# Kernel tuning notes

Hardware: AMD Instinct MI355X
Metric: run time of the kernel (lower is better)

The kernel has to match this reference:

```python
import jax, jax.numpy as jnp
import numpy as np

BATCH, SEQ_LEN, VEC_DIM, WIDTH = 64, 256, 512, 3


def setup_inputs() -> dict:
    key = jax.random.key(0)
    k = jax.random.split(key, 8)
    F0r = jax.random.normal(k[0], (BATCH, SEQ_LEN, VEC_DIM), jnp.float32)
    F1r = jax.random.normal(k[1], (BATCH, SEQ_LEN, VEC_DIM), jnp.float32)
    sent0_mask = (jax.random.uniform(k[2], (BATCH, SEQ_LEN)) < 0.9).astype(jnp.float32)
    sent1_mask = (jax.random.uniform(k[3], (BATCH, SEQ_LEN)) < 0.9).astype(jnp.float32)
    # nn.Parameter(torch.randn(seq_len, vec_dim))
    W0 = jax.random.normal(k[4], (SEQ_LEN, VEC_DIM), jnp.float32)
    W1 = jax.random.normal(k[5], (SEQ_LEN, VEC_DIM), jnp.float32)
    # Conv2d(2, 1, kernel_size=(WIDTH, 1)) default init: U(-1/sqrt(fan_in), +)
    bound = 1.0 / np.sqrt(2 * WIDTH * 1)
    conv_w = jax.random.uniform(k[6], (1, 2, WIDTH, 1), jnp.float32, -bound, bound)
    conv_b = jax.random.uniform(k[7], (1,), jnp.float32, -bound, bound)
    return dict(F0r=F0r, F1r=F1r, sent0_mask=sent0_mask, sent1_mask=sent1_mask,
                W0=W0, W1=W1, conv_w=conv_w, conv_b=conv_b)


def _conv_tanh_pool(x, conv_w, conv_b):
    # x: [B, 2, S, D]; conv pad (WIDTH-1, 0) -> [B, 1, S+WIDTH-1, D]
    y = jax.lax.conv_general_dilated(
        x, conv_w, window_strides=(1, 1),
        padding=((WIDTH - 1, WIDTH - 1), (0, 0)),
        dimension_numbers=('NCHW', 'OIHW', 'NCHW'))
    y = jnp.tanh(y + conv_b[None, :, None, None])
    # AvgPool2d kernel (WIDTH,1), stride 1 -> [B, 1, S, D]
    y = jax.lax.reduce_window(y, 0.0, jax.lax.add,
                              (1, 1, WIDTH, 1), (1, 1, 1, 1), 'VALID') / WIDTH
    return y[:, 0]  # squeeze channel -> [B, S, D]


def reference(F0r, F1r, sent0_mask, sent1_mask, W0, W1, conv_w, conv_b):
    # masking is in-place in the torch code, so masked F0/F1 feed the conv too
    F0 = F0r * sent0_mask[:, :, None]  # [B, S, D]
    F1 = F1r * sent1_mask[:, :, None]
    # pairwise L2 via ||u-v||^2 = ||u||^2 + ||v||^2 - 2 u.v (avoids [B,S,S,D])
    sq0 = jnp.sum(F0 * F0, axis=-1)  # [B, S]
    sq1 = jnp.sum(F1 * F1, axis=-1)
    cross = jnp.einsum('bid,bjd->bij', F0, F1)  # [B, S, S]
    d2 = jnp.maximum(sq0[:, :, None] + sq1[:, None, :] - 2.0 * cross, 0.0)
    norm = jnp.where(d2 > 0, jnp.sqrt(jnp.where(d2 > 0, d2, 1.0)), 0.0)
    A = 1.0 / (1.0 + norm)  # [B, S, S]
    F0a = jnp.einsum('bij,id->bjd', A, W0)  # A^T @ W0
    F1a = jnp.einsum('bij,jd->bid', A, W1)  # A @ W1
    x0 = jnp.stack([F0, F0a], axis=1)  # [B, 2, S, D]
    x1 = jnp.stack([F1, F1a], axis=1)
    out0 = _conv_tanh_pool(x0, conv_w, conv_b)
    out1 = _conv_tanh_pool(x1, conv_w, conv_b)
    return out0, out1
```

## Files before the change

kernel.cpp:

```cpp
#include <hip/hip_runtime.h>

typedef unsigned short u16;
typedef __attribute__((ext_vector_type(8))) short short8;
typedef __attribute__((ext_vector_type(4))) float f32x4;

__device__ inline u16 f2bf(float f) {
    union { float f; unsigned u; } v; v.f = f;
    unsigned u = v.u;
    unsigned r = (u + 0x7FFFu + ((u >> 16) & 1u)) >> 16;
    return (u16)r;
}
__device__ inline float bf2f(u16 h) {
    union { unsigned u; float f; } v; v.u = ((unsigned)h) << 16;
    return v.f;
}
__device__ inline float ftanh(float x) {
    float e = __expf(2.f * x);
    return 1.f - 2.f / (e + 1.f);
}

__global__ __launch_bounds__(128) void prep_kernel(
    const float* __restrict__ F0r, const float* __restrict__ F1r,
    const float* __restrict__ m0, const float* __restrict__ m1,
    u16* __restrict__ F0b, u16* __restrict__ F1b,
    float* __restrict__ sq0, float* __restrict__ sq1)
{
    int bs = blockIdx.x;
    int t = threadIdx.x;
    size_t base = (size_t)bs * 512 + t * 4;
    float mk0 = m0[bs], mk1 = m1[bs];
    float4 v0 = *(const float4*)(F0r + base);
    float4 v1 = *(const float4*)(F1r + base);
    v0.x *= mk0; v0.y *= mk0; v0.z *= mk0; v0.w *= mk0;
    v1.x *= mk1; v1.y *= mk1; v1.z *= mk1; v1.w *= mk1;
    ushort4 u0; u0.x = f2bf(v0.x); u0.y = f2bf(v0.y); u0.z = f2bf(v0.z); u0.w = f2bf(v0.w);
    ushort4 u1; u1.x = f2bf(v1.x); u1.y = f2bf(v1.y); u1.z = f2bf(v1.z); u1.w = f2bf(v1.w);
    *(ushort4*)(F0b + base) = u0;
    *(ushort4*)(F1b + base) = u1;
    float s0p = v0.x*v0.x + v0.y*v0.y + v0.z*v0.z + v0.w*v0.w;
    float s1p = v1.x*v1.x + v1.y*v1.y + v1.z*v1.z + v1.w*v1.w;
    #pragma unroll
    for (int off = 32; off > 0; off >>= 1) {
        s0p += __shfl_xor(s0p, off);
        s1p += __shfl_xor(s1p, off);
    }
    __shared__ float red0[2], red1[2];
    if ((t & 63) == 0) { red0[t >> 6] = s0p; red1[t >> 6] = s1p; }
    __syncthreads();
    if (t == 0) { sq0[bs] = red0[0] + red0[1]; sq1[bs] = red1[0] + red1[1]; }
}

__global__ __launch_bounds__(256) void wtrans_kernel(
    const float* __restrict__ W0, const float* __restrict__ W1,
    u16* __restrict__ WT0, u16* __restrict__ WT1)
{
    int idx = blockIdx.x * 256 + threadIdx.x;
    int a = idx >> 17;
    int r = idx & 131071;
    int s = r >> 9, d = r & 511;
    const float* W = a ? W1 : W0;
    u16* WT = a ? WT1 : WT0;
    WT[d * 256 + s] = f2bf(W[r]);
}

__device__ inline void gemm128_core(
    const u16* __restrict__ Ap, int lda,
    const u16* __restrict__ Bp, int ldb,
    int K, int m0, int n0,
    u16 (*As)[72], u16 (*Bs)[72],
    f32x4 acc[4][4])
{
    const int t = threadIdx.x;
    const int lane = t & 63, w = t >> 6;
    const int wm = w >> 1, wn = w & 1;
    const int q = lane >> 4, lm = lane & 15;

    for (int k0 = 0; k0 < K; k0 += 64) {
        #pragma unroll
        for (int i = 0; i < 4; ++i) {
            int idx = i * 256 + t;
            int row = idx >> 3;
            int seg = idx & 7;
            *(uint4*)&As[row][seg * 8] =
                *(const uint4*)(Ap + (size_t)(m0 + row) * lda + k0 + seg * 8);
            *(uint4*)&Bs[row][seg * 8] =
                *(const uint4*)(Bp + (size_t)(n0 + row) * ldb + k0 + seg * 8);
        }
        __syncthreads();
        #pragma unroll
        for (int ks = 0; ks < 64; ks += 32) {
            short8 af[4], bfr[4];
            #pragma unroll
            for (int x = 0; x < 4; ++x) {
                af[x]  = *(const short8*)&As[wm * 64 + x * 16 + lm][ks + q * 8];
                bfr[x] = *(const short8*)&Bs[wn * 64 + x * 16 + lm][ks + q * 8];
            }
            #pragma unroll
            for (int x = 0; x < 4; ++x)
                #pragma unroll
                for (int y = 0; y < 4; ++y)
                    acc[x][y] = __builtin_amdgcn_mfma_f32_16x16x32_bf16(
                        af[x], bfr[y], acc[x][y], 0, 0, 0);
        }
        __syncthreads();
    }
}

__global__ __launch_bounds__(256) void gemm_cross_kernel(
    const u16* __restrict__ F0b, const u16* __restrict__ F1b,
    const float* __restrict__ sq0, const float* __restrict__ sq1,
    u16* __restrict__ Abf, u16* __restrict__ ATbf)
{
    __shared__ __align__(16) u16 As[128][72];
    __shared__ __align__(16) u16 Bs[128][72];
    int b = blockIdx.y, var = blockIdx.z;
    int m0 = (blockIdx.x >> 1) * 128, n0 = (blockIdx.x & 1) * 128;
    const u16 *Ap, *Bp; const float *sqR, *sqC; u16* Out;
    if (var == 0) {
        Ap = F0b + (size_t)b * 131072; Bp = F1b + (size_t)b * 131072;
        sqR = sq0 + b * 256; sqC = sq1 + b * 256;
        Out = Abf + (size_t)b * 65536;
    } else {
        Ap = F1b + (size_t)b * 131072; Bp = F0b + (size_t)b * 131072;
        sqR = sq1 + b * 256; sqC = sq0 + b * 256;
        Out = ATbf + (size_t)b * 65536;
    }
    f32x4 acc[4][4];
    #pragma unroll
    for (int x = 0; x < 4; ++x)
        #pragma unroll
        for (int y = 0; y < 4; ++y)
            acc[x][y] = (f32x4){0.f, 0.f, 0.f, 0.f};

    gemm128_core(Ap, 512, Bp, 512, 512, m0, n0, As, Bs, acc);

    const int t = threadIdx.x;
    const int lane = t & 63, w = t >> 6;
    const int wm = w >> 1, wn = w & 1, q = lane >> 4, lm = lane & 15;
    #pragma unroll
    for (int x = 0; x < 4; ++x) {
        #pragma unroll
        for (int r = 0; r < 4; ++r) {
            int i = m0 + wm * 64 + x * 16 + q * 4 + r;
            float si = sqR[i];
            #pragma unroll
            for (int y = 0; y < 4; ++y) {
                int j = n0 + wn * 64 + y * 16 + lm;
                float c = acc[x][y][r];
                float d2 = si + sqC[j] - 2.f * c;
                d2 = fmaxf(d2, 0.f);
                float a = 1.f / (1.f + sqrtf(d2));
                Out[(size_t)i * 256 + j] = f2bf(a);
            }
        }
    }
}

__global__ __launch_bounds__(256) void gemm_fa_kernel(
    const u16* __restrict__ Abf, const u16* __restrict__ ATbf,
    const u16* __restrict__ WT0, const u16* __restrict__ WT1,
    u16* __restrict__ F0a, u16* __restrict__ F1a)
{
    __shared__ __align__(16) u16 As[128][72];
    __shared__ __align__(16) u16 Bs[128][72];
    int b = blockIdx.y, var = blockIdx.z;
    int m0 = (blockIdx.x >> 2) * 128;
    int n0 = (blockIdx.x & 3) * 128;
    const u16 *Ap, *Bp; u16* Out;
    if (var == 0) { Ap = ATbf + (size_t)b * 65536; Bp = WT0; Out = F0a + (size_t)b * 131072; }
    else          { Ap = Abf  + (size_t)b * 65536; Bp = WT1; Out = F1a + (size_t)b * 131072; }
    f32x4 acc[4][4];
    #pragma unroll
    for (int x = 0; x < 4; ++x)
        #pragma unroll
        for (int y = 0; y < 4; ++y)
            acc[x][y] = (f32x4){0.f, 0.f, 0.f, 0.f};

    gemm128_core(Ap, 256, Bp, 256, 256, m0, n0, As, Bs, acc);

    const int t = threadIdx.x;
    const int lane = t & 63, w = t >> 6;
    const int wm = w >> 1, wn = w & 1, q = lane >> 4, lm = lane & 15;
    #pragma unroll
    for (int x = 0; x < 4; ++x) {
        #pragma unroll
        for (int r = 0; r < 4; ++r) {
            int row = m0 + wm * 64 + x * 16 + q * 4 + r;
            #pragma unroll
            for (int y = 0; y < 4; ++y) {
                int col = n0 + wn * 64 + y * 16 + lm;
                Out[(size_t)row * 512 + col] = f2bf(acc[x][y][r]);
            }
        }
    }
}

__device__ inline void load_row_cv(
    const float* __restrict__ Fr, const float* __restrict__ mask,
    const u16* __restrict__ Fa, int s, int d0, float4& f, float4& a)
{
    if ((unsigned)s < 256u) {
        float4 v = *(const float4*)(Fr + (size_t)s * 512 + d0);
        float m = mask[s];
        f.x = v.x * m; f.y = v.y * m; f.z = v.z * m; f.w = v.w * m;
        ushort4 u = *(const ushort4*)(Fa + (size_t)s * 512 + d0);
        a.x = bf2f(u.x); a.y = bf2f(u.y); a.z = bf2f(u.z); a.w = bf2f(u.w);
    } else {
        f = make_float4(0.f, 0.f, 0.f, 0.f);
        a = make_float4(0.f, 0.f, 0.f, 0.f);
    }
}

__global__ __launch_bounds__(128) void conv_kernel(
    const float* __restrict__ F0r, const float* __restrict__ F1r,
    const float* __restrict__ m0, const float* __restrict__ m1,
    const u16* __restrict__ F0a, const u16* __restrict__ F1a,
    const float* __restrict__ cw, const float* __restrict__ cb,
    float* __restrict__ out)
{
    int b = blockIdx.y;
    int which = blockIdx.z;
    int s0 = blockIdx.x * 16;
    int d0 = threadIdx.x * 4;
    const float* Fr = (which ? F1r : F0r) + (size_t)b * 131072;
    const float* mask = (which ? m1 : m0) + b * 256;
    const u16* Fa = (which ? F1a : F0a) + (size_t)b * 131072;
    float* o = out + (size_t)which * 8388608 + (size_t)b * 131072 + d0;
    float w00 = cw[0], w01 = cw[1], w02 = cw[2];
    float w10 = cw[3], w11 = cw[4], w12 = cw[5];
    float bias = cb[0];

    float4 fm2, fm1, fc, fp1, fp2, am2, am1, ac, ap1, ap2;
    load_row_cv(Fr, mask, Fa, s0 - 2, d0, fm2, am2);
    load_row_cv(Fr, mask, Fa, s0 - 1, d0, fm1, am1);
    load_row_cv(Fr, mask, Fa, s0,     d0, fc,  ac);
    load_row_cv(Fr, mask, Fa, s0 + 1, d0, fp1, ap1);
    load_row_cv(Fr, mask, Fa, s0 + 2, d0, fp2, ap2);

    #define CONV_Y(Y, F0_, F1_, F2_, A0_, A1_, A2_)                                \
        { Y.x = bias + w00*F0_.x + w01*F1_.x + w02*F2_.x + w10*A0_.x + w11*A1_.x + w12*A2_.x; \
          Y.y = bias + w00*F0_.y + w01*F1_.y + w02*F2_.y + w10*A0_.y + w11*A1_.y + w12*A2_.y; \
          Y.z = bias + w00*F0_.z + w01*F1_.z + w02*F2_.z + w10*A0_.z + w11*A1_.z + w12*A2_.z; \
          Y.w = bias + w00*F0_.w + w01*F1_.w + w02*F2_.w + w10*A0_.w + w11*A1_.w + w12*A2_.w; }
    #define TANH4(Y) { Y.x = ftanh(Y.x); Y.y = ftanh(Y.y); Y.z = ftanh(Y.z); Y.w = ftanh(Y.w); }

    float4 ty0, ty1;
    CONV_Y(ty0, fm2, fm1, fc, am2, am1, ac); TANH4(ty0);
    CONV_Y(ty1, fm1, fc, fp1, am1, ac, ap1); TANH4(ty1);

    float4 w0f = fc, w1f = fp1, w2f = fp2;
    float4 w0a = ac, w1a = ap1, w2a = ap2;
    const float third = 1.f / 3.f;
    for (int s = s0; s < s0 + 16; ++s) {
        float4 ty2;
        CONV_Y(ty2, w0f, w1f, w2f, w0a, w1a, w2a); TANH4(ty2);
        float4 r;
        r.x = (ty0.x + ty1.x + ty2.x) * third;
        r.y = (ty0.y + ty1.y + ty2.y) * third;
        r.z = (ty0.z + ty1.z + ty2.z) * third;
        r.w = (ty0.w + ty1.w + ty2.w) * third;
        *(float4*)(o + (size_t)s * 512) = r;
        ty0 = ty1; ty1 = ty2;
        w0f = w1f; w1f = w2f;
        w0a = w1a; w1a = w2a;
        load_row_cv(Fr, mask, Fa, s + 3, d0, w2f, w2a);
    }
    #undef CONV_Y
    #undef TANH4
}

extern "C" void kernel_launch(void* const* d_in, const int* in_sizes, int n_in,
                              void* d_out, int out_size, void* d_ws, size_t ws_size,
                              hipStream_t stream)
{
    const float* F0r = (const float*)d_in[0];
    const float* F1r = (const float*)d_in[1];
    const float* m0  = (const float*)d_in[2];
    const float* m1  = (const float*)d_in[3];
    const float* W0  = (const float*)d_in[4];
    const float* W1  = (const float*)d_in[5];
    const float* cw  = (const float*)d_in[6];
    const float* cb  = (const float*)d_in[7];
    float* out = (float*)d_out;

    char* ws = (char*)d_ws;
    u16* F0b   = (u16*)(ws);
    u16* F1b   = (u16*)(ws + 16777216);
    u16* Abf   = (u16*)(ws + 33554432);
    u16* ATbf  = (u16*)(ws + 41943040);
    float* sq0 = (float*)(ws + 50331648);
    float* sq1 = (float*)(ws + 50397184);
    u16* WT0   = (u16*)(ws + 50462720);
    u16* WT1   = (u16*)(ws + 50724864);
    u16* F0a = F0b;
    u16* F1a = F1b;

    prep_kernel<<<16384, 128, 0, stream>>>(F0r, F1r, m0, m1, F0b, F1b, sq0, sq1);
    wtrans_kernel<<<1024, 256, 0, stream>>>(W0, W1, WT0, WT1);
    gemm_cross_kernel<<<dim3(4, 64, 2), 256, 0, stream>>>(F0b, F1b, sq0, sq1, Abf, ATbf);
    gemm_fa_kernel<<<dim3(8, 64, 2), 256, 0, stream>>>(Abf, ATbf, WT0, WT1, F0a, F1a);
    conv_kernel<<<dim3(16, 64, 2), 128, 0, stream>>>(F0r, F1r, m0, m1, F0a, F1a, cw, cb, out);
}
```

Baseline: 202.2 us.

## Compute cross distance once, write A and transpose via LDS, shrink GEMM tiles

The cross-distance GEMM used to be run twice, once for A and once for A^T. It now runs once per batch tile, stages the bf16 result in shared memory, and writes both A and its transpose from that tile with vectorized stores. Both GEMM kernels move from 128x128 to 64x64 tiles, which gives more blocks and fills more CUs. The epilogues are restaged through LDS so global writes are coalesced. In exchange, the smaller tiles give less data reuse per block, and the transposed reads from LDS may hit bank conflicts.

```diff
diff --git a/kernel.cpp b/kernel.cpp
--- a/kernel.cpp
+++ b/kernel.cpp
@@ -63,42 +63,42 @@
     WT[d * 256 + s] = f2bf(W[r]);
 }
 
-__device__ inline void gemm128_core(
+__device__ inline void gemm64_core(
     const u16* __restrict__ Ap, int lda,
     const u16* __restrict__ Bp, int ldb,
     int K, int m0, int n0,
     u16 (*As)[72], u16 (*Bs)[72],
-    f32x4 acc[4][4])
+    f32x4 acc[2][2])
 {
     const int t = threadIdx.x;
     const int lane = t & 63, w = t >> 6;
     const int wm = w >> 1, wn = w & 1;
     const int q = lane >> 4, lm = lane & 15;
+    const int srow = t >> 3;
+    const int sseg = t & 7;
 
     for (int k0 = 0; k0 < K; k0 += 64) {
         #pragma unroll
-        for (int i = 0; i < 4; ++i) {
-            int idx = i * 256 + t;
-            int row = idx >> 3;
-            int seg = idx & 7;
-            *(uint4*)&As[row][seg * 8] =
-                *(const uint4*)(Ap + (size_t)(m0 + row) * lda + k0 + seg * 8);
-            *(uint4*)&Bs[row][seg * 8] =
-                *(const uint4*)(Bp + (size_t)(n0 + row) * ldb + k0 + seg * 8);
+        for (int i = 0; i < 2; ++i) {
+            int row = i * 32 + srow;
+            *(uint4*)&As[row][sseg * 8] =
+                *(const uint4*)(Ap + (size_t)(m0 + row) * lda + k0 + sseg * 8);
+            *(uint4*)&Bs[row][sseg * 8] =
+                *(const uint4*)(Bp + (size_t)(n0 + row) * ldb + k0 + sseg * 8);
         }
         __syncthreads();
         #pragma unroll
         for (int ks = 0; ks < 64; ks += 32) {
-            short8 af[4], bfr[4];
+            short8 af[2], bfr[2];
             #pragma unroll
-            for (int x = 0; x < 4; ++x) {
-                af[x]  = *(const short8*)&As[wm * 64 + x * 16 + lm][ks + q * 8];
-                bfr[x] = *(const short8*)&Bs[wn * 64 + x * 16 + lm][ks + q * 8];
+            for (int x = 0; x < 2; ++x) {
+                af[x]  = *(const short8*)&As[wm * 32 + x * 16 + lm][ks + q * 8];
+                bfr[x] = *(const short8*)&Bs[wn * 32 + x * 16 + lm][ks + q * 8];
             }
             #pragma unroll
-            for (int x = 0; x < 4; ++x)
+            for (int x = 0; x < 2; ++x)
                 #pragma unroll
-                for (int y = 0; y < 4; ++y)
+                for (int y = 0; y < 2; ++y)
                     acc[x][y] = __builtin_amdgcn_mfma_f32_16x16x32_bf16(
                         af[x], bfr[y], acc[x][y], 0, 0, 0);
         }
@@ -111,48 +111,63 @@
     const float* __restrict__ sq0, const float* __restrict__ sq1,
     u16* __restrict__ Abf, u16* __restrict__ ATbf)
 {
-    __shared__ __align__(16) u16 As[128][72];
-    __shared__ __align__(16) u16 Bs[128][72];
-    int b = blockIdx.y, var = blockIdx.z;
-    int m0 = (blockIdx.x >> 1) * 128, n0 = (blockIdx.x & 1) * 128;
-    const u16 *Ap, *Bp; const float *sqR, *sqC; u16* Out;
-    if (var == 0) {
-        Ap = F0b + (size_t)b * 131072; Bp = F1b + (size_t)b * 131072;
-        sqR = sq0 + b * 256; sqC = sq1 + b * 256;
-        Out = Abf + (size_t)b * 65536;
-    } else {
-        Ap = F1b + (size_t)b * 131072; Bp = F0b + (size_t)b * 131072;
-        sqR = sq1 + b * 256; sqC = sq0 + b * 256;
-        Out = ATbf + (size_t)b * 65536;
-    }
-    f32x4 acc[4][4];
-    #pragma unroll
-    for (int x = 0; x < 4; ++x)
-        #pragma unroll
-        for (int y = 0; y < 4; ++y)
+    __shared__ __align__(16) u16 As[64][72];
+    __shared__ __align__(16) u16 Bs[64][72];
+    int b = blockIdx.y;
+    int i0 = (blockIdx.x >> 2) * 64, j0 = (blockIdx.x & 3) * 64;
+    const u16* Ap = F0b + (size_t)b * 131072;
+    const u16* Bp = F1b + (size_t)b * 131072;
+    const float* sqR = sq0 + b * 256;
+    const float* sqC = sq1 + b * 256;
+
+    f32x4 acc[2][2];
+    #pragma unroll
+    for (int x = 0; x < 2; ++x)
+        #pragma unroll
+        for (int y = 0; y < 2; ++y)
             acc[x][y] = (f32x4){0.f, 0.f, 0.f, 0.f};
 
-    gemm128_core(Ap, 512, Bp, 512, 512, m0, n0, As, Bs, acc);
+    gemm64_core(Ap, 512, Bp, 512, 512, i0, j0, As, Bs, acc);
 
     const int t = threadIdx.x;
     const int lane = t & 63, w = t >> 6;
     const int wm = w >> 1, wn = w & 1, q = lane >> 4, lm = lane & 15;
-    #pragma unroll
-    for (int x = 0; x < 4; ++x) {
+    u16 (*Ct)[72] = As;
+    #pragma unroll
+    for (int x = 0; x < 2; ++x) {
         #pragma unroll
         for (int r = 0; r < 4; ++r) {
-            int i = m0 + wm * 64 + x * 16 + q * 4 + r;
-            float si = sqR[i];
+            int ir = wm * 32 + x * 16 + q * 4 + r;
+            float si = sqR[i0 + ir];
             #pragma unroll
-            for (int y = 0; y < 4; ++y) {
-                int j = n0 + wn * 64 + y * 16 + lm;
-                float c = acc[x][y][r];
-                float d2 = si + sqC[j] - 2.f * c;
+            for (int y = 0; y < 2; ++y) {
+                int jc = wn * 32 + y * 16 + lm;
+                float d2 = si + sqC[j0 + jc] - 2.f * acc[x][y][r];
                 d2 = fmaxf(d2, 0.f);
                 float a = 1.f / (1.f + sqrtf(d2));
-                Out[(size_t)i * 256 + j] = f2bf(a);
+                Ct[ir][jc] = f2bf(a);
             }
         }
+    }
+    __syncthreads();
+
+    u16* Aout  = Abf  + (size_t)b * 65536;
+    u16* ATout = ATbf + (size_t)b * 65536;
+    int ii = t >> 2;
+    int c0 = (t & 3) * 16;
+    #pragma unroll
+    for (int c = 0; c < 4; ++c) {
+        ushort4 v = *(ushort4*)&Ct[ii][c0 + c * 4];
+        *(ushort4*)&Aout[(size_t)(i0 + ii) * 256 + j0 + c0 + c * 4] = v;
+    }
+    #pragma unroll
+    for (int c = 0; c < 4; ++c) {
+        ushort4 v;
+        v.x = Ct[c0 + c * 4 + 0][ii];
+        v.y = Ct[c0 + c * 4 + 1][ii];
+        v.z = Ct[c0 + c * 4 + 2][ii];
+        v.w = Ct[c0 + c * 4 + 3][ii];
+        *(ushort4*)&ATout[(size_t)(j0 + ii) * 256 + i0 + c0 + c * 4] = v;
     }
 }
 
@@ -161,37 +176,46 @@
     const u16* __restrict__ WT0, const u16* __restrict__ WT1,
     u16* __restrict__ F0a, u16* __restrict__ F1a)
 {
-    __shared__ __align__(16) u16 As[128][72];
-    __shared__ __align__(16) u16 Bs[128][72];
+    __shared__ __align__(16) u16 As[64][72];
+    __shared__ __align__(16) u16 Bs[64][72];
     int b = blockIdx.y, var = blockIdx.z;
-    int m0 = (blockIdx.x >> 2) * 128;
-    int n0 = (blockIdx.x & 3) * 128;
+    int m0 = (blockIdx.x >> 3) * 64;
+    int n0 = (blockIdx.x & 7) * 64;
     const u16 *Ap, *Bp; u16* Out;
     if (var == 0) { Ap = ATbf + (size_t)b * 65536; Bp = WT0; Out = F0a + (size_t)b * 131072; }
     else          { Ap = Abf  + (size_t)b * 65536; Bp = WT1; Out = F1a + (size_t)b * 131072; }
-    f32x4 acc[4][4];
-    #pragma unroll
-    for (int x = 0; x < 4; ++x)
-        #pragma unroll
-        for (int y = 0; y < 4; ++y)
+
+    f32x4 acc[2][2];
+    #pragma unroll
+    for (int x = 0; x < 2; ++x)
+        #pragma unroll
+        for (int y = 0; y < 2; ++y)
             acc[x][y] = (f32x4){0.f, 0.f, 0.f, 0.f};
 
-    gemm128_core(Ap, 256, Bp, 256, 256, m0, n0, As, Bs, acc);
+    gemm64_core(Ap, 256, Bp, 256, 256, m0, n0, As, Bs, acc);
 
     const int t = threadIdx.x;
     const int lane = t & 63, w = t >> 6;
     const int wm = w >> 1, wn = w & 1, q = lane >> 4, lm = lane & 15;
-    #pragma unroll
-    for (int x = 0; x < 4; ++x) {
+    u16 (*Ct)[72] = As;
+    #pragma unroll
+    for (int x = 0; x < 2; ++x)
         #pragma unroll
         for (int r = 0; r < 4; ++r) {
-            int row = m0 + wm * 64 + x * 16 + q * 4 + r;
+            int ir = wm * 32 + x * 16 + q * 4 + r;
             #pragma unroll
-            for (int y = 0; y < 4; ++y) {
-                int col = n0 + wn * 64 + y * 16 + lm;
-                Out[(size_t)row * 512 + col] = f2bf(acc[x][y][r]);
+            for (int y = 0; y < 2; ++y) {
+                int jc = wn * 32 + y * 16 + lm;
+                Ct[ir][jc] = f2bf(acc[x][y][r]);
             }
         }
+    __syncthreads();
+    int ii = t >> 2;
+    int c0 = (t & 3) * 16;
+    #pragma unroll
+    for (int c = 0; c < 4; ++c) {
+        ushort4 v = *(ushort4*)&Ct[ii][c0 + c * 4];
+        *(ushort4*)&Out[(size_t)(m0 + ii) * 512 + n0 + c0 + c * 4] = v;
     }
 }
 
@@ -297,7 +321,7 @@
 
     prep_kernel<<<16384, 128, 0, stream>>>(F0r, F1r, m0, m1, F0b, F1b, sq0, sq1);
     wtrans_kernel<<<1024, 256, 0, stream>>>(W0, W1, WT0, WT1);
-    gemm_cross_kernel<<<dim3(4, 64, 2), 256, 0, stream>>>(F0b, F1b, sq0, sq1, Abf, ATbf);
-    gemm_fa_kernel<<<dim3(8, 64, 2), 256, 0, stream>>>(Abf, ATbf, WT0, WT1, F0a, F1a);
+    gemm_cross_kernel<<<dim3(16, 64), 256, 0, stream>>>(F0b, F1b, sq0, sq1, Abf, ATbf);
+    gemm_fa_kernel<<<dim3(32, 64, 2), 256, 0, stream>>>(Abf, ATbf, WT0, WT1, F0a, F1a);
     conv_kernel<<<dim3(16, 64, 2), 128, 0, stream>>>(F0r, F1r, m0, m1, F0a, F1a, cw, cb, out);
 }
```

Result: slower. 208.3 us (+3.0%).
